# Optimization experiments

Measured on AMD Instinct MI355X. Metric: run time of the kernel, lower is better.

The kernel has to match this reference:

```python
import jax, jax.numpy as jnp
import numpy as np


def setup_inputs() -> dict:
    key = jax.random.key(0)
    k1, k2 = jax.random.split(key)
    B, N, D = 32, 8192, 128
    queries = jax.random.normal(k1, (B, 1, D), dtype=jnp.float32)
    values = jax.random.normal(k2, (B, N, D), dtype=jnp.float32)
    return {"queries": queries, "values": values}


def reference(queries, values):
    # scores: bmm(q [B,1,D], v^T [B,D,N]) -> [B,1,N] -> squeeze -> [B,N]
    scores = jnp.einsum("bqd,bnd->bn", queries, values)
    attn = jax.nn.softmax(scores, axis=-1)            # [B, N]
    # weighted sum over N; no explicit repeat needed (broadcast instead)
    context = jnp.einsum("bn,bnd->bd", attn, values)  # [B, D]
    return (attn, context)
```

## Files before the change

kernel.cpp:

```cpp
#include <hip/hip_runtime.h>
#include <hip/hip_bf16.h>
#include <math.h>

#define B 32
#define NROWS 8192
#define D 128
#define CHUNK 256
#define NCHUNK (NROWS / CHUNK)
#define NWAVES 8
#define RPW (CHUNK / NWAVES)
#define NIT (RPW / 4)
#define SHIFT 16.0f

template <int CTRL>
__device__ __forceinline__ float dpp_add(float x) {
    int y = __builtin_amdgcn_update_dpp(
        0, __float_as_int(x), CTRL, 0xf, 0xf, true);
    return x + __int_as_float(y);
}

__device__ __forceinline__ void half_reduce(float p, float& s_lo, float& s_hi) {
    p = dpp_add<0x111>(p);
    p = dpp_add<0x112>(p);
    p = dpp_add<0x114>(p);
    p = dpp_add<0x118>(p);
    p = dpp_add<0x142>(p);
    s_lo = __int_as_float(__builtin_amdgcn_readlane(__float_as_int(p), 31));
    s_hi = __int_as_float(__builtin_amdgcn_readlane(__float_as_int(p), 63));
}

__global__ __launch_bounds__(512) void attend_k1(
    const float* __restrict__ q,
    const float* __restrict__ v,
    float* __restrict__ out_scores,
    float* __restrict__ part_l,
    float* __restrict__ part_o)
{
    __shared__ float s_sc[CHUNK];
    __shared__ float wl8[NWAVES];
    __shared__ float wo[NWAVES][D];

    const int b    = blockIdx.x >> 5;
    const int c    = blockIdx.x & (NCHUNK - 1);
    const int n0   = c * CHUNK;
    const int tid  = threadIdx.x;
    const int w    = tid >> 6;
    const int lane = tid & 63;
    const int half = lane >> 5;
    const int l32  = lane & 31;

    const float4 q4 = ((const float4*)(q + b * D))[l32];
    const float4* vb = (const float4*)(v + ((size_t)b * NROWS + n0 + w * RPW) * D);

    float l = 0.f;
    float4 acc = make_float4(0.f, 0.f, 0.f, 0.f);

    float4 a0 = vb[lane];
    float4 a1 = vb[64 + lane];

    #pragma unroll 2
    for (int i = 0; i < NIT; ++i) {
        const int j = (i + 1 < NIT) ? i + 1 : i;
        const float4 b0 = vb[j * 128 + lane];
        const float4 b1 = vb[j * 128 + 64 + lane];

        float p0 = a0.x * q4.x + a0.y * q4.y + a0.z * q4.z + a0.w * q4.w;
        float p1 = a1.x * q4.x + a1.y * q4.y + a1.z * q4.z + a1.w * q4.w;

        float s0lo, s0hi, s1lo, s1hi;
        half_reduce(p0, s0lo, s0hi);
        half_reduce(p1, s1lo, s1hi);
        const float s0 = half ? s0hi : s0lo;
        const float s1 = half ? s1hi : s1lo;
        if (l32 == 0) {
            s_sc[w * RPW + 4 * i + half]     = s0;
            s_sc[w * RPW + 4 * i + 2 + half] = s1;
        }

        const float e0 = __expf(s0 - SHIFT);
        const float e1 = __expf(s1 - SHIFT);
        l += e0 + e1;
        acc.x += e0 * a0.x + e1 * a1.x;
        acc.y += e0 * a0.y + e1 * a1.y;
        acc.z += e0 * a0.z + e1 * a1.z;
        acc.w += e0 * a0.w + e1 * a1.w;

        a0 = b0; a1 = b1;
    }

    l += __shfl_xor(l, 32, 64);
    acc.x += __shfl_xor(acc.x, 32, 64);
    acc.y += __shfl_xor(acc.y, 32, 64);
    acc.z += __shfl_xor(acc.z, 32, 64);
    acc.w += __shfl_xor(acc.w, 32, 64);
    if (half == 0) {
        ((float4*)wo[w])[l32] = acc;
        if (l32 == 0) wl8[w] = l;
    }
    __syncthreads();

    if (tid < CHUNK)
        out_scores[(size_t)b * NROWS + n0 + tid] = s_sc[tid];

    if (tid < D) {
        float o = 0.f;
        #pragma unroll
        for (int ww = 0; ww < NWAVES; ++ww) o += wo[ww][tid];
        part_o[(size_t)blockIdx.x * D + tid] = o;
        if (tid == 0) {
            float L = 0.f;
            #pragma unroll
            for (int ww = 0; ww < NWAVES; ++ww) L += wl8[ww];
            part_l[blockIdx.x] = L;
        }
    }
}

__global__ __launch_bounds__(128) void attend_k2(
    const float* __restrict__ part_l,
    const float* __restrict__ part_o,
    float* __restrict__ out_ctx,
    float* __restrict__ bInvL)
{
    const int b = blockIdx.x;
    const int d = threadIdx.x;

    float L = 0.f, o = 0.f;
    #pragma unroll
    for (int c = 0; c < NCHUNK; ++c) {
        L += part_l[b * NCHUNK + c];
        o += part_o[(size_t)(b * NCHUNK + c) * D + d];
    }
    out_ctx[b * D + d] = o / L;
    if (d == 0) bInvL[b] = 1.0f / L;
}

__global__ __launch_bounds__(256) void attend_k3(
    float* __restrict__ attn,
    const float* __restrict__ bInvL)
{
    const int idx = blockIdx.x * 256 + threadIdx.x;
    const int b   = idx >> 11;
    const float invL = bInvL[b];
    float4 s = ((float4*)attn)[idx];
    s.x = __expf(s.x - SHIFT) * invL;
    s.y = __expf(s.y - SHIFT) * invL;
    s.z = __expf(s.z - SHIFT) * invL;
    s.w = __expf(s.w - SHIFT) * invL;
    ((float4*)attn)[idx] = s;
}

extern "C" void kernel_launch(void* const* d_in, const int* in_sizes, int n_in,
                              void* d_out, int out_size, void* d_ws, size_t ws_size,
                              hipStream_t stream) {
    const float* q = (const float*)d_in[0];
    const float* v = (const float*)d_in[1];
    float* out = (float*)d_out;

    float* ws      = (float*)d_ws;
    float* part_l  = ws;
    float* part_o  = part_l + B * NCHUNK;
    float* bInvL   = part_o + (size_t)B * NCHUNK * D;

    attend_k1<<<B * NCHUNK, 512, 0, stream>>>(q, v, out, part_l, part_o);
    attend_k2<<<B, 128, 0, stream>>>(part_l, part_o, out + (size_t)B * NROWS, bInvL);
    attend_k3<<<(B * NROWS / 4) / 256, 256, 0, stream>>>(out, bInvL);
}
```

Baseline: 196.6 us.

## Store exponentials in main pass, fuse normalization kernels, use nontemporal value loads

The chunk kernel now writes the shifted exponentials instead of raw scores. That removes the exp recomputation from the final pass. The reduce kernel and the attention-normalize kernel are merged into one launch of 32 blocks, which drops a launch and the inverse-sum round trip through memory, but the normalization pass now runs with far fewer blocks. The streaming value reads use nontemporal loads so they do less damage to the cache.

```diff
diff --git a/kernel.cpp b/kernel.cpp
--- a/kernel.cpp
+++ b/kernel.cpp
@@ -11,6 +11,11 @@
 #define RPW (CHUNK / NWAVES)
 #define NIT (RPW / 4)
 #define SHIFT 16.0f
+
+typedef float v4f __attribute__((ext_vector_type(4)));
+__device__ __forceinline__ v4f nt_load4(const v4f* p) {
+    return __builtin_nontemporal_load(p);
+}
 
 template <int CTRL>
 __device__ __forceinline__ float dpp_add(float x) {
@@ -32,7 +37,7 @@
 __global__ __launch_bounds__(512) void attend_k1(
     const float* __restrict__ q,
     const float* __restrict__ v,
-    float* __restrict__ out_scores,
+    float* __restrict__ out_e,
     float* __restrict__ part_l,
     float* __restrict__ part_o)
 {
@@ -50,19 +55,19 @@
     const int l32  = lane & 31;
 
     const float4 q4 = ((const float4*)(q + b * D))[l32];
-    const float4* vb = (const float4*)(v + ((size_t)b * NROWS + n0 + w * RPW) * D);
+    const v4f* vb = (const v4f*)(v + ((size_t)b * NROWS + n0 + w * RPW) * D);
 
     float l = 0.f;
     float4 acc = make_float4(0.f, 0.f, 0.f, 0.f);
 
-    float4 a0 = vb[lane];
-    float4 a1 = vb[64 + lane];
+    v4f a0 = nt_load4(vb + lane);
+    v4f a1 = nt_load4(vb + 64 + lane);
 
     #pragma unroll 2
     for (int i = 0; i < NIT; ++i) {
         const int j = (i + 1 < NIT) ? i + 1 : i;
-        const float4 b0 = vb[j * 128 + lane];
-        const float4 b1 = vb[j * 128 + 64 + lane];
+        const v4f b0 = nt_load4(vb + j * 128 + lane);
+        const v4f b1 = nt_load4(vb + j * 128 + 64 + lane);
 
         float p0 = a0.x * q4.x + a0.y * q4.y + a0.z * q4.z + a0.w * q4.w;
         float p1 = a1.x * q4.x + a1.y * q4.y + a1.z * q4.z + a1.w * q4.w;
@@ -72,13 +77,13 @@
         half_reduce(p1, s1lo, s1hi);
         const float s0 = half ? s0hi : s0lo;
         const float s1 = half ? s1hi : s1lo;
-        if (l32 == 0) {
-            s_sc[w * RPW + 4 * i + half]     = s0;
-            s_sc[w * RPW + 4 * i + 2 + half] = s1;
-        }
 
         const float e0 = __expf(s0 - SHIFT);
         const float e1 = __expf(s1 - SHIFT);
+        if (l32 == 0) {
+            s_sc[w * RPW + 4 * i + half]     = e0;
+            s_sc[w * RPW + 4 * i + 2 + half] = e1;
+        }
         l += e0 + e1;
         acc.x += e0 * a0.x + e1 * a1.x;
         acc.y += e0 * a0.y + e1 * a1.y;
@@ -100,7 +105,7 @@
     __syncthreads();
 
     if (tid < CHUNK)
-        out_scores[(size_t)b * NROWS + n0 + tid] = s_sc[tid];
+        out_e[(size_t)b * NROWS + n0 + tid] = s_sc[tid];
 
     if (tid < D) {
         float o = 0.f;
@@ -116,38 +121,34 @@
     }
 }
 
-__global__ __launch_bounds__(128) void attend_k2(
+__global__ __launch_bounds__(256) void attend_k2(
     const float* __restrict__ part_l,
     const float* __restrict__ part_o,
-    float* __restrict__ out_ctx,
-    float* __restrict__ bInvL)
+    float* __restrict__ out)
 {
-    const int b = blockIdx.x;
-    const int d = threadIdx.x;
+    const int b   = blockIdx.x;
+    const int tid = threadIdx.x;
 
-    float L = 0.f, o = 0.f;
+    float L = 0.f;
     #pragma unroll
-    for (int c = 0; c < NCHUNK; ++c) {
-        L += part_l[b * NCHUNK + c];
-        o += part_o[(size_t)(b * NCHUNK + c) * D + d];
+    for (int c = 0; c < NCHUNK; ++c) L += part_l[b * NCHUNK + c];
+    const float invL = 1.0f / L;
+
+    if (tid < D) {
+        float o = 0.f;
+        #pragma unroll
+        for (int c = 0; c < NCHUNK; ++c)
+            o += part_o[(size_t)(b * NCHUNK + c) * D + tid];
+        out[(size_t)B * NROWS + b * D + tid] = o * invL;
     }
-    out_ctx[b * D + d] = o / L;
-    if (d == 0) bInvL[b] = 1.0f / L;
-}
 
-__global__ __launch_bounds__(256) void attend_k3(
-    float* __restrict__ attn,
-    const float* __restrict__ bInvL)
-{
-    const int idx = blockIdx.x * 256 + threadIdx.x;
-    const int b   = idx >> 11;
-    const float invL = bInvL[b];
-    float4 s = ((float4*)attn)[idx];
-    s.x = __expf(s.x - SHIFT) * invL;
-    s.y = __expf(s.y - SHIFT) * invL;
-    s.z = __expf(s.z - SHIFT) * invL;
-    s.w = __expf(s.w - SHIFT) * invL;
-    ((float4*)attn)[idx] = s;
+    float4* attn4 = (float4*)(out + (size_t)b * NROWS);
+    #pragma unroll
+    for (int i = 0; i < (NROWS / 4) / 256; ++i) {
+        float4 s = attn4[i * 256 + tid];
+        s.x *= invL; s.y *= invL; s.z *= invL; s.w *= invL;
+        attn4[i * 256 + tid] = s;
+    }
 }
 
 extern "C" void kernel_launch(void* const* d_in, const int* in_sizes, int n_in,
@@ -160,9 +161,7 @@
     float* ws      = (float*)d_ws;
     float* part_l  = ws;
     float* part_o  = part_l + B * NCHUNK;
-    float* bInvL   = part_o + (size_t)B * NCHUNK * D;
 
     attend_k1<<<B * NCHUNK, 512, 0, stream>>>(q, v, out, part_l, part_o);
-    attend_k2<<<B, 128, 0, stream>>>(part_l, part_o, out + (size_t)B * NROWS, bInvL);
-    attend_k3<<<(B * NROWS / 4) / 256, 256, 0, stream>>>(out, bInvL);
+    attend_k2<<<B, 256, 0, stream>>>(part_l, part_o, out);
 }
```

After: 184.4 us. -6.2%, faster.
